# Kernel optimization log

Hardware: AMD Instinct MI355X
Metric: run time of the kernel (lower is better)

## Reference

```python
import jax, jax.numpy as jnp
import numpy as np

B, N, D, NUM_K = 128, 1024, 64, 8


def setup_inputs() -> dict:
    key = jax.random.key(0)
    k1, k2, k3 = jax.random.split(key, 3)
    nodes = jax.random.normal(k1, (B, N, D), dtype=jnp.float32)
    # xavier_uniform over (in_dims, in_dims) fan: bound = sqrt(6 / (N + N))
    bound = float(np.sqrt(6.0 / (N + N)))
    weight = jax.random.uniform(k2, (NUM_K, N, N), dtype=jnp.float32,
                                minval=-bound, maxval=bound)
    graph_shift = jax.random.normal(k3, (N, N), dtype=jnp.float32) / np.sqrt(N)
    return {"nodes": nodes, "weight": weight, "graph_shift": graph_shift}


def reference(nodes, weight, graph_shift):
    """Polynomial graph filter: out[b] = sum_k W_k @ S^k @ X_b.

    Since sum_k W_k S^k X = (sum_k W_k S^k) X, we fuse all taps into one
    N x N operator A, then apply a single batched GEMM over the batch.
    """
    n = nodes.shape[1]
    eye = jnp.eye(n, dtype=nodes.dtype)

    def step(S, Wk):
        # emit W_k @ S^k, carry S^{k+1}
        return S @ graph_shift, Wk @ S

    _, Mk = jax.lax.scan(step, eye, weight)   # [num_k, N, N]
    A = Mk.sum(axis=0)                        # fused filter operator [N, N]
    return jnp.einsum('nm,bmd->bnd', A, nodes)  # [B, N, D]
```

## Files before the change

### kernel.cpp

```cpp
#include <hip/hip_runtime.h>
#include <stdint.h>


#define NN 1024
#define NBATCH 128
#define DDIM 64

typedef float floatx16 __attribute__((ext_vector_type(16)));
typedef _Float16 f16x8 __attribute__((ext_vector_type(8)));
typedef unsigned short u16;

__device__ __forceinline__ u16 f2h(float f) {
  union { _Float16 h; u16 u; } v; v.h = (_Float16)f; return v.u;
}
__device__ __forceinline__ float h2f(u16 u) {
  union { _Float16 h; u16 u; } v; v.u = u; return (float)v.h;
}

__device__ __forceinline__ void gll16(const void* g, void* l) {
  __builtin_amdgcn_global_load_lds(
      (const __attribute__((address_space(1))) void*)g,
      (__attribute__((address_space(3))) void*)l, 16, 0, 0);
}

template <int ROWS>
__device__ __forceinline__ void stage64(const u16* __restrict__ g, u16* lds,
                                        int wave, int lane) {
  const int r = lane >> 3, c = lane & 7;
  const int sw = (c ^ r) * 8;
#pragma unroll
  for (int i = 0; i < ROWS / 32; ++i) {
    const int rb = wave * (ROWS / 4) + i * 8;
    gll16(g + (size_t)(rb + r) * NN + sw, lds + rb * 64);
  }
}

__device__ __forceinline__ f16x8 frag(const u16* lds, int r, int ks, int half) {
  return *(const f16x8*)&lds[r * 64 + (((ks * 2 + half) ^ (r & 7)) * 8)];
}

struct CvtJob { const float* src; u16* rm; u16* cm; };
struct CvtJobs { CvtJob j[5]; };

__global__ __launch_bounds__(256) void cvt_kernel(CvtJobs jobs) {
  CvtJob jb = jobs.j[blockIdx.z];
  int idx4 = blockIdx.x * 256 + threadIdx.x;
  int e = idx4 * 4;
  int row = e >> 10, col = e & (NN - 1);
  float4 f = ((const float4*)jb.src)[idx4];
  u16 h[4] = { f2h(f.x), f2h(f.y), f2h(f.z), f2h(f.w) };
  uint2 p;
  p.x = (uint32_t)h[0] | ((uint32_t)h[1] << 16);
  p.y = (uint32_t)h[2] | ((uint32_t)h[3] << 16);
  *(uint2*)&jb.rm[e] = p;
  if (jb.cm) {
#pragma unroll
    for (int i = 0; i < 4; ++i) jb.cm[(size_t)(col + i) * NN + row] = h[i];
  }
}

__global__ __launch_bounds__(256) void transpose_x(const float* __restrict__ X,
                                                   u16* __restrict__ XT) {
  __shared__ u16 T[64][72];
  const int k0 = blockIdx.x * 64;
  const int b = blockIdx.y;
  const int t = threadIdx.x;
#pragma unroll
  for (int it = 0; it < 4; ++it) {
    int kr = (t >> 4) + it * 16;
    int d4 = (t & 15) * 4;
    float4 f = *(const float4*)&X[((size_t)b * NN + k0 + kr) * DDIM + d4];
    T[d4 + 0][kr] = f2h(f.x);
    T[d4 + 1][kr] = f2h(f.y);
    T[d4 + 2][kr] = f2h(f.z);
    T[d4 + 3][kr] = f2h(f.w);
  }
  __syncthreads();
#pragma unroll
  for (int it = 0; it < 2; ++it) {
    int d = (t >> 3) + it * 32;
    int kc = (t & 7) * 8;
    *(uint4*)&XT[((size_t)b * DDIM + d) * NN + k0 + kc] = *(uint4*)&T[d][kc];
  }
}

struct GemmJob {
  const u16* A;
  const u16* B;
  const float* addF;
  const u16* addH;
  u16* outRm;
  u16* outCm;
  float* outP;
};
struct GemmJobs { GemmJob j[5]; };

template <int BM, int BN, int KSPLIT>
__global__ __launch_bounds__(256) void gemm_f16(GemmJobs jobs) {
  const GemmJob jb = jobs.j[blockIdx.z / KSPLIT];
  const int chunk = blockIdx.z % KSPLIT;
  __shared__ u16 As[BM * 64], Bs[BN * 64];
  const int t = threadIdx.x, wave = t >> 6, lane = t & 63;
  const int wm = wave >> 1, wn = wave & 1;
  const int l31 = lane & 31, half = lane >> 5;
  const int bm = blockIdx.x * BM, bn = blockIdx.y * BN;
  constexpr int MI = BM / 64, NI = BN / 64, KTPB = 16 / KSPLIT;
  floatx16 acc[MI][NI] = {};

  for (int kk = 0; kk < KTPB; ++kk) {
    const int kt = chunk * KTPB + kk;
    __syncthreads();
    stage64<BM>(jb.A + (size_t)bm * NN + kt * 64, As, wave, lane);
    stage64<BN>(jb.B + (size_t)bn * NN + kt * 64, Bs, wave, lane);
    __syncthreads();
#pragma unroll
    for (int ks = 0; ks < 4; ++ks) {
      f16x8 bf[NI];
#pragma unroll
      for (int ni = 0; ni < NI; ++ni)
        bf[ni] = frag(Bs, wn * (BN / 2) + ni * 32 + l31, ks, half);
#pragma unroll
      for (int mi = 0; mi < MI; ++mi) {
        f16x8 a = frag(As, wm * (BM / 2) + mi * 32 + l31, ks, half);
#pragma unroll
        for (int ni = 0; ni < NI; ++ni)
          acc[mi][ni] = __builtin_amdgcn_mfma_f32_32x32x16_f16(a, bf[ni], acc[mi][ni], 0, 0, 0);
      }
    }
  }

#pragma unroll
  for (int mi = 0; mi < MI; ++mi)
#pragma unroll
    for (int ni = 0; ni < NI; ++ni)
#pragma unroll
      for (int r = 0; r < 16; ++r) {
        int row = bm + wm * (BM / 2) + mi * 32 + (r & 3) + 8 * (r >> 2) + 4 * half;
        int col = bn + wn * (BN / 2) + ni * 32 + l31;
        size_t rm = (size_t)row * NN + col;
        float v = acc[mi][ni][r];
        if (KSPLIT > 1) {
          jb.outP[(size_t)chunk * NN * NN + rm] = v;
        } else {
          if (jb.addF) v += jb.addF[rm];
          if (jb.addH) v += h2f(jb.addH[rm]);
          u16 h = f2h(v);
          if (jb.outRm) jb.outRm[rm] = h;
          if (jb.outCm) jb.outCm[(size_t)col * NN + row] = h;
        }
      }
}

__global__ __launch_bounds__(256) void combine_A(const float* __restrict__ parts,
                                                 const u16* __restrict__ v0,
                                                 u16* __restrict__ A) {
  int e = (blockIdx.x * 256 + threadIdx.x) * 4;
  float4 s = *(const float4*)&parts[e];
#pragma unroll
  for (int z = 1; z < 4; ++z) {
    float4 p = *(const float4*)&parts[(size_t)z * NN * NN + e];
    s.x += p.x; s.y += p.y; s.z += p.z; s.w += p.w;
  }
  uint2 h = *(const uint2*)&v0[e];
  uint2 o;
  o.x = (uint32_t)f2h(s.x + h2f((u16)h.x)) |
        ((uint32_t)f2h(s.y + h2f((u16)(h.x >> 16))) << 16);
  o.y = (uint32_t)f2h(s.z + h2f((u16)h.y)) |
        ((uint32_t)f2h(s.w + h2f((u16)(h.y >> 16))) << 16);
  *(uint2*)&A[e] = o;
}

__global__ __launch_bounds__(256) void apply_gemm(const u16* __restrict__ A,
                                                  const u16* __restrict__ XT,
                                                  float* __restrict__ out) {
  __shared__ u16 As[8192], Xs[4096];
  const int t = threadIdx.x, wave = t >> 6, lane = t & 63;
  const int l31 = lane & 31, half = lane >> 5;
  const int b = blockIdx.x, bm = blockIdx.y * 128;
  floatx16 acc[2] = {};

  for (int kt = 0; kt < 16; ++kt) {
    __syncthreads();
    stage64<128>(A + (size_t)bm * NN + kt * 64, As, wave, lane);
    stage64<64>(XT + (size_t)b * DDIM * NN + kt * 64, Xs, wave, lane);
    __syncthreads();
#pragma unroll
    for (int ks = 0; ks < 4; ++ks) {
      f16x8 a = frag(As, wave * 32 + l31, ks, half);
#pragma unroll
      for (int ni = 0; ni < 2; ++ni) {
        f16x8 x = frag(Xs, ni * 32 + l31, ks, half);
        acc[ni] = __builtin_amdgcn_mfma_f32_32x32x16_f16(a, x, acc[ni], 0, 0, 0);
      }
    }
  }

#pragma unroll
  for (int ni = 0; ni < 2; ++ni)
#pragma unroll
    for (int r = 0; r < 16; ++r) {
      int row = bm + wave * 32 + (r & 3) + 8 * (r >> 2) + 4 * half;
      int d = ni * 32 + l31;
      out[((size_t)b * NN + row) * DDIM + d] = acc[ni][r];
    }
}

extern "C" void kernel_launch(void* const* d_in, const int* in_sizes, int n_in,
                              void* d_out, int out_size, void* d_ws, size_t ws_size,
                              hipStream_t stream) {
  const float* nodes  = (const float*)d_in[0];
  const float* weight = (const float*)d_in[1];
  const float* gs     = (const float*)d_in[2];
  float* out = (float*)d_out;
  u16* ws = (u16*)d_ws;
  const size_t MB = (size_t)NN * NN;
  auto buf = [&](int i) -> u16* { return ws + (size_t)i * MB; };

  CvtJobs cv{};
  cv.j[0] = { gs,              buf(0), buf(1) };
  cv.j[1] = { weight + 1 * MB, buf(2), nullptr };
  cv.j[2] = { weight + 3 * MB, buf(3), nullptr };
  cv.j[3] = { weight + 5 * MB, buf(4), nullptr };
  cv.j[4] = { weight + 7 * MB, buf(5), nullptr };
  cvt_kernel<<<dim3(NN * NN / 1024, 1, 5), 256, 0, stream>>>(cv);

  GemmJobs g1{};
  g1.j[0] = { buf(0), buf(1), nullptr,         nullptr, buf(6),  buf(7),  nullptr };
  g1.j[1] = { buf(2), buf(1), weight + 0 * MB, nullptr, buf(8),  nullptr, nullptr };
  g1.j[2] = { buf(3), buf(1), weight + 2 * MB, nullptr, buf(9),  nullptr, nullptr };
  g1.j[3] = { buf(4), buf(1), weight + 4 * MB, nullptr, buf(10), nullptr, nullptr };
  g1.j[4] = { buf(5), buf(1), weight + 6 * MB, nullptr, buf(11), nullptr, nullptr };
  gemm_f16<64, 128, 1><<<dim3(16, 8, 5), 256, 0, stream>>>(g1);

  u16* XT = buf(16);
  transpose_x<<<dim3(16, NBATCH), 256, 0, stream>>>(nodes, XT);

  GemmJobs g2{};
  g2.j[0] = { buf(6),  buf(7), nullptr, nullptr, nullptr, buf(12), nullptr };
  g2.j[1] = { buf(9),  buf(7), nullptr, buf(8),  buf(13), nullptr, nullptr };
  g2.j[2] = { buf(11), buf(7), nullptr, buf(10), buf(14), nullptr, nullptr };
  gemm_f16<64, 64, 1><<<dim3(16, 16, 3), 256, 0, stream>>>(g2);

  float* parts = (float*)buf(24);
  GemmJobs g3{};
  g3.j[0] = { buf(14), buf(12), nullptr, nullptr, nullptr, nullptr, parts };
  gemm_f16<64, 64, 4><<<dim3(16, 16, 4), 256, 0, stream>>>(g3);

  combine_A<<<dim3(NN * NN / 1024), 256, 0, stream>>>(parts, buf(13), buf(15));

  apply_gemm<<<dim3(NBATCH, 8), 256, 0, stream>>>(buf(15), XT, out);
}
```

Measured before the change: 205.0 us.

## Stage LDS tiles in MFMA fragment order and merge prep kernels

```diff
diff --git a/kernel.cpp b/kernel.cpp
--- a/kernel.cpp
+++ b/kernel.cpp
@@ -24,52 +24,52 @@
 }
 
 template <int ROWS>
-__device__ __forceinline__ void stage64(const u16* __restrict__ g, u16* lds,
-                                        int wave, int lane) {
-  const int r = lane >> 3, c = lane & 7;
-  const int sw = (c ^ r) * 8;
+__device__ __forceinline__ void stageF(const u16* __restrict__ g, u16* lds,
+                                       int wave, int lane) {
+  const int r = lane & 31, h = lane >> 5;
 #pragma unroll
   for (int i = 0; i < ROWS / 32; ++i) {
-    const int rb = wave * (ROWS / 4) + i * 8;
-    gll16(g + (size_t)(rb + r) * NN + sw, lds + rb * 64);
-  }
-}
-
-__device__ __forceinline__ f16x8 frag(const u16* lds, int r, int ks, int half) {
-  return *(const f16x8*)&lds[r * 64 + (((ks * 2 + half) ^ (r & 7)) * 8)];
+    const int o = wave + i * 4;
+    const int j = o >> 2, ks = o & 3;
+    gll16(g + (size_t)(j * 32 + r) * NN + (ks * 2 + h) * 8,
+          lds + j * 2048 + ks * 512);
+  }
+}
+
+__device__ __forceinline__ f16x8 fragF(const u16* lds, int j, int ks, int lane) {
+  return *(const f16x8*)&lds[j * 2048 + ks * 512 + lane * 8];
 }
 
 struct CvtJob { const float* src; u16* rm; u16* cm; };
-struct CvtJobs { CvtJob j[5]; };
-
-__global__ __launch_bounds__(256) void cvt_kernel(CvtJobs jobs) {
-  CvtJob jb = jobs.j[blockIdx.z];
-  int idx4 = blockIdx.x * 256 + threadIdx.x;
-  int e = idx4 * 4;
-  int row = e >> 10, col = e & (NN - 1);
-  float4 f = ((const float4*)jb.src)[idx4];
-  u16 h[4] = { f2h(f.x), f2h(f.y), f2h(f.z), f2h(f.w) };
-  uint2 p;
-  p.x = (uint32_t)h[0] | ((uint32_t)h[1] << 16);
-  p.y = (uint32_t)h[2] | ((uint32_t)h[3] << 16);
-  *(uint2*)&jb.rm[e] = p;
-  if (jb.cm) {
-#pragma unroll
-    for (int i = 0; i < 4; ++i) jb.cm[(size_t)(col + i) * NN + row] = h[i];
-  }
-}
-
-__global__ __launch_bounds__(256) void transpose_x(const float* __restrict__ X,
-                                                   u16* __restrict__ XT) {
+struct PrepArgs { CvtJob cv[5]; const float* X; u16* XT; };
+
+__global__ __launch_bounds__(256) void prep_kernel(PrepArgs pa) {
+  const int z = blockIdx.z, x = blockIdx.x, t = threadIdx.x;
+  if (z < 5) {
+    if (x >= NN * NN / 1024) return;
+    CvtJob jb = pa.cv[z];
+    int idx4 = x * 256 + t;
+    int e = idx4 * 4;
+    int row = e >> 10, col = e & (NN - 1);
+    float4 f = ((const float4*)jb.src)[idx4];
+    u16 h[4] = { f2h(f.x), f2h(f.y), f2h(f.z), f2h(f.w) };
+    uint2 p;
+    p.x = (uint32_t)h[0] | ((uint32_t)h[1] << 16);
+    p.y = (uint32_t)h[2] | ((uint32_t)h[3] << 16);
+    *(uint2*)&jb.rm[e] = p;
+    if (jb.cm) {
+#pragma unroll
+      for (int i = 0; i < 4; ++i) jb.cm[(size_t)(col + i) * NN + row] = h[i];
+    }
+    return;
+  }
   __shared__ u16 T[64][72];
-  const int k0 = blockIdx.x * 64;
-  const int b = blockIdx.y;
-  const int t = threadIdx.x;
+  const int k0 = (x & 15) * 64, b = x >> 4;
 #pragma unroll
   for (int it = 0; it < 4; ++it) {
     int kr = (t >> 4) + it * 16;
     int d4 = (t & 15) * 4;
-    float4 f = *(const float4*)&X[((size_t)b * NN + k0 + kr) * DDIM + d4];
+    float4 f = *(const float4*)&pa.X[((size_t)b * NN + k0 + kr) * DDIM + d4];
     T[d4 + 0][kr] = f2h(f.x);
     T[d4 + 1][kr] = f2h(f.y);
     T[d4 + 2][kr] = f2h(f.z);
@@ -80,7 +80,7 @@
   for (int it = 0; it < 2; ++it) {
     int d = (t >> 3) + it * 32;
     int kc = (t & 7) * 8;
-    *(uint4*)&XT[((size_t)b * DDIM + d) * NN + k0 + kc] = *(uint4*)&T[d][kc];
+    *(uint4*)&pa.XT[((size_t)b * DDIM + d) * NN + k0 + kc] = *(uint4*)&T[d][kc];
   }
 }
 
@@ -110,18 +110,18 @@
   for (int kk = 0; kk < KTPB; ++kk) {
     const int kt = chunk * KTPB + kk;
     __syncthreads();
-    stage64<BM>(jb.A + (size_t)bm * NN + kt * 64, As, wave, lane);
-    stage64<BN>(jb.B + (size_t)bn * NN + kt * 64, Bs, wave, lane);
+    stageF<BM>(jb.A + (size_t)bm * NN + kt * 64, As, wave, lane);
+    stageF<BN>(jb.B + (size_t)bn * NN + kt * 64, Bs, wave, lane);
     __syncthreads();
 #pragma unroll
     for (int ks = 0; ks < 4; ++ks) {
       f16x8 bf[NI];
 #pragma unroll
       for (int ni = 0; ni < NI; ++ni)
-        bf[ni] = frag(Bs, wn * (BN / 2) + ni * 32 + l31, ks, half);
+        bf[ni] = fragF(Bs, wn * (BN / 64) + ni, ks, lane);
 #pragma unroll
       for (int mi = 0; mi < MI; ++mi) {
-        f16x8 a = frag(As, wm * (BM / 2) + mi * 32 + l31, ks, half);
+        f16x8 a = fragF(As, wm * (BM / 64) + mi, ks, lane);
 #pragma unroll
         for (int ni = 0; ni < NI; ++ni)
           acc[mi][ni] = __builtin_amdgcn_mfma_f32_32x32x16_f16(a, bf[ni], acc[mi][ni], 0, 0, 0);
@@ -181,15 +181,15 @@
 
   for (int kt = 0; kt < 16; ++kt) {
     __syncthreads();
-    stage64<128>(A + (size_t)bm * NN + kt * 64, As, wave, lane);
-    stage64<64>(XT + (size_t)b * DDIM * NN + kt * 64, Xs, wave, lane);
+    stageF<128>(A + (size_t)bm * NN + kt * 64, As, wave, lane);
+    stageF<64>(XT + (size_t)b * DDIM * NN + kt * 64, Xs, wave, lane);
     __syncthreads();
 #pragma unroll
     for (int ks = 0; ks < 4; ++ks) {
-      f16x8 a = frag(As, wave * 32 + l31, ks, half);
+      f16x8 a = fragF(As, wave, ks, lane);
 #pragma unroll
       for (int ni = 0; ni < 2; ++ni) {
-        f16x8 x = frag(Xs, ni * 32 + l31, ks, half);
+        f16x8 x = fragF(Xs, ni, ks, lane);
         acc[ni] = __builtin_amdgcn_mfma_f32_32x32x16_f16(a, x, acc[ni], 0, 0, 0);
       }
     }
@@ -216,13 +216,15 @@
   const size_t MB = (size_t)NN * NN;
   auto buf = [&](int i) -> u16* { return ws + (size_t)i * MB; };
 
-  CvtJobs cv{};
-  cv.j[0] = { gs,              buf(0), buf(1) };
-  cv.j[1] = { weight + 1 * MB, buf(2), nullptr };
-  cv.j[2] = { weight + 3 * MB, buf(3), nullptr };
-  cv.j[3] = { weight + 5 * MB, buf(4), nullptr };
-  cv.j[4] = { weight + 7 * MB, buf(5), nullptr };
-  cvt_kernel<<<dim3(NN * NN / 1024, 1, 5), 256, 0, stream>>>(cv);
+  u16* XT = buf(16);
+  PrepArgs pa{};
+  pa.cv[0] = { gs,              buf(0), buf(1) };
+  pa.cv[1] = { weight + 1 * MB, buf(2), nullptr };
+  pa.cv[2] = { weight + 3 * MB, buf(3), nullptr };
+  pa.cv[3] = { weight + 5 * MB, buf(4), nullptr };
+  pa.cv[4] = { weight + 7 * MB, buf(5), nullptr };
+  pa.X = nodes; pa.XT = XT;
+  prep_kernel<<<dim3(16 * NBATCH, 1, 6), 256, 0, stream>>>(pa);
 
   GemmJobs g1{};
   g1.j[0] = { buf(0), buf(1), nullptr,         nullptr, buf(6),  buf(7),  nullptr };
@@ -232,9 +234,6 @@
   g1.j[4] = { buf(5), buf(1), weight + 6 * MB, nullptr, buf(11), nullptr, nullptr };
   gemm_f16<64, 128, 1><<<dim3(16, 8, 5), 256, 0, stream>>>(g1);
 
-  u16* XT = buf(16);
-  transpose_x<<<dim3(16, NBATCH), 256, 0, stream>>>(nodes, XT);
-
   GemmJobs g2{};
   g2.j[0] = { buf(6),  buf(7), nullptr, nullptr, nullptr, buf(12), nullptr };
   g2.j[1] = { buf(9),  buf(7), nullptr, buf(8),  buf(13), nullptr, nullptr };
```

New measurement: 255.7 us. +24.8%, slower.
